# Optimization experiments

Hardware: AMD Instinct MI355X
Metric: run time of the kernel (lower is better)

## Reference

```python
import jax, jax.numpy as jnp
import numpy as np

N_NODES = 50000
N_EDGES = 800000
N_GRAPHS = 64
HID = 128
FEAT = 64
OUT = 32
N_LAYERS = 3
DECAY = 0.9
THRESH = 0.1


def setup_inputs() -> dict:
    key = jax.random.key(0)
    ks = jax.random.split(key, 24)
    s = 0.05
    inp = {
        "x": jax.random.normal(ks[0], (N_NODES, FEAT), jnp.float32),
        "edge_attr": jax.random.normal(ks[1], (N_EDGES, 1), jnp.float32),
        "initial_importance": jax.random.uniform(ks[2], (N_NODES, 1), jnp.float32),
        "imp_proj_W": jax.random.normal(ks[3], (1, HID), jnp.float32) * s,
        "imp_proj_b": jnp.zeros((HID,), jnp.float32),
        "init_W": jax.random.normal(ks[4], (FEAT + HID, HID), jnp.float32) * s,
        "init_b": jnp.zeros((HID,), jnp.float32),
        "msg_W": jax.random.normal(ks[5], (N_LAYERS, HID, HID), jnp.float32) * s,
        "msg_b": jnp.zeros((N_LAYERS, HID), jnp.float32),
        "upd_W": jax.random.normal(ks[6], (N_LAYERS, 2 * HID, HID), jnp.float32) * s,
        "upd_b": jnp.zeros((N_LAYERS, HID), jnp.float32),
        "gate_W": jax.random.normal(ks[7], (N_LAYERS, HID + 1, HID), jnp.float32) * s,
        "gate_b": jnp.zeros((N_LAYERS, HID), jnp.float32),
        "prop_W": jax.random.normal(ks[8], (N_LAYERS, HID, 1), jnp.float32) * s,
        "prop_b": jnp.zeros((N_LAYERS, 1), jnp.float32),
        "norm_w": jnp.ones((N_LAYERS, HID), jnp.float32),
        "norm_b": jnp.zeros((N_LAYERS, HID), jnp.float32),
        "norm_a": jnp.ones((N_LAYERS, HID), jnp.float32),
        "final_W": jax.random.normal(ks[9], (HID, OUT), jnp.float32) * s,
        "final_b": jnp.zeros((OUT,), jnp.float32),
        "edge_index": jax.random.randint(ks[10], (2, N_EDGES), 0, N_NODES, jnp.int32),
        # evenly spread sorted graph ids -> every graph non-empty
        "batch": (jnp.arange(N_NODES, dtype=jnp.int32) * N_GRAPHS) // N_NODES,
    }
    return inp


def _normalize_importance(imp, batch):
    # per-graph min/max normalization, fused segment reductions
    mn = jax.ops.segment_min(imp, batch, num_segments=N_GRAPHS)[batch]
    mx = jax.ops.segment_max(imp, batch, num_segments=N_GRAPHS)[batch]
    return (imp - mn) / (mx - mn + 1e-8)


def _graph_norm(x, batch, counts, w, b, a):
    # PyG GraphNorm: y = w * (x - a*mean) / sqrt(var(x - a*mean) + eps) + b
    mean = jax.ops.segment_sum(x, batch, num_segments=N_GRAPHS) / counts
    out = x - a * mean[batch]
    var = jax.ops.segment_sum(out * out, batch, num_segments=N_GRAPHS) / counts
    std = jnp.sqrt(var + 1e-5)
    return w * out / std[batch] + b


def _forward(x, edge_attr, initial_importance, imp_proj_W, imp_proj_b, init_W,
             init_b, msg_W, msg_b, upd_W, upd_b, gate_W, gate_b, prop_W, prop_b,
             norm_w, norm_b, norm_a, final_W, final_b, edge_index, batch):
    src, dst = edge_index[0], edge_index[1]
    counts = jax.ops.segment_sum(jnp.ones((N_NODES, 1), x.dtype), batch,
                                 num_segments=N_GRAPHS)  # [G,1]

    imp0 = initial_importance[:, 0]                       # [N]
    importance = _normalize_importance(imp0, batch)       # [N]
    imp_emb = importance[:, None] @ imp_proj_W + imp_proj_b  # [N,H]
    h = jnp.concatenate([x, imp_emb], axis=-1) @ init_W + init_b  # [N,H]

    for l in range(N_LAYERS):
        # MPNN: gather -> linear -> scatter-add -> update
        msg = h[src] @ msg_W[l] + msg_b[l]                # [E,H]
        aggr = jax.ops.segment_sum(msg, dst, num_segments=N_NODES)  # [N,H]
        conv = jnp.concatenate([h, aggr], axis=-1) @ upd_W[l] + upd_b[l]
        # importance gating
        gate_in = jnp.concatenate([conv, importance[:, None]], axis=-1)
        gate = jax.nn.sigmoid(gate_in @ gate_W[l] + gate_b[l])
        out = gate * conv + (1.0 - gate) * h
        prop = out @ prop_W[l] + prop_b[l]                # [N,1]
        # norm + relu (dropout p=0 in eval)
        h = jax.nn.relu(_graph_norm(out, batch, counts, norm_w[l], norm_b[l], norm_a[l]))
        # importance update
        imp = DECAY * importance + (1.0 - DECAY) * prop[:, 0]
        imp = _normalize_importance(imp, batch)
        imp = jnp.where(imp < THRESH, 0.0, imp)
        importance = _normalize_importance(imp, batch)

    h = h @ final_W + final_b                             # [N,OUT]
    logits = jax.ops.segment_sum(h, batch, num_segments=N_GRAPHS) / counts  # [G,OUT]
    final_importance = _normalize_importance(imp0 + importance, batch)
    return logits, final_importance[:, None]


def reference(x, edge_attr, initial_importance, imp_proj_W, imp_proj_b, init_W,
              init_b, msg_W, msg_b, upd_W, upd_b, gate_W, gate_b, prop_W, prop_b,
              norm_w, norm_b, norm_a, final_W, final_b, edge_index, batch):
    return _forward(x, edge_attr, initial_importance, imp_proj_W, imp_proj_b,
                    init_W, init_b, msg_W, msg_b, upd_W, upd_b, gate_W, gate_b,
                    prop_W, prop_b, norm_w, norm_b, norm_a, final_W, final_b,
                    edge_index, batch)
```

## Files before the change

### kernel.cpp

```cpp
#include <hip/hip_runtime.h>
#include <cstdint>

#define NN 50000
#define NE 800000
#define NG 64
#define HD 128
#define FT 64
#define NLAYERS 3
#define MB 32
#define NBLK 1563
#define AGN 64
#define AGB (8*((NN + AGN - 1)/AGN))

__global__ void k_gbounds(const int* __restrict__ batch, int* __restrict__ gstart){
    int i = blockIdx.x*blockDim.x + threadIdx.x;
    if (i >= NN) return;
    int g = batch[i];
    if (i == 0){ for (int q = 0; q <= g; ++q) gstart[q] = 0; }
    else { int gp = batch[i-1]; for (int q = gp+1; q <= g; ++q) gstart[q] = i; }
    if (i == NN-1){ for (int q = g+1; q <= NG; ++q) gstart[q] = NN; }
}

__device__ __forceinline__ void block_minmax(float lmn, float lmx, float* red,
                                             float& omn, float& omx){
    #pragma unroll
    for (int off = 32; off > 0; off >>= 1){
        lmn = fminf(lmn, __shfl_xor(lmn, off));
        lmx = fmaxf(lmx, __shfl_xor(lmx, off));
    }
    int wave = threadIdx.x >> 6;
    if ((threadIdx.x & 63) == 0){ red[wave] = lmn; red[4+wave] = lmx; }
    __syncthreads();
    omn = fminf(fminf(red[0], red[1]), fminf(red[2], red[3]));
    omx = fmaxf(fmaxf(red[4], red[5]), fmaxf(red[6], red[7]));
    __syncthreads();
}

__global__ __launch_bounds__(256) void k_norm_graph(
    const float* __restrict__ va, const int* __restrict__ gstart,
    float* __restrict__ out)
{
    __shared__ float sv[1024];
    __shared__ float red[8];
    int g = blockIdx.x;
    int s = gstart[g], n = gstart[g+1] - s;
    int tid = threadIdx.x;
    float lmn = 3.4e38f, lmx = -3.4e38f;
    for (int i = tid; i < n; i += 256){
        float v = va[s+i];
        sv[i] = v;
        lmn = fminf(lmn, v); lmx = fmaxf(lmx, v);
    }
    float lo, hi;
    block_minmax(lmn, lmx, red, lo, hi);
    float inv = 1.f/(hi - lo + 1e-8f);
    for (int i = tid; i < n; i += 256) out[s+i] = (sv[i] - lo)*inv;
}

__global__ void k_fold_init(const float* __restrict__ pW, const float* __restrict__ pb,
                            const float* __restrict__ iW, const float* __restrict__ ib,
                            float* __restrict__ W0, float* __restrict__ b0){
    int j = threadIdx.x;
    for (int k = 0; k < FT; ++k) W0[k*HD + j] = iW[k*HD + j];
    float w2 = 0.f, b2 = 0.f;
    for (int k = 0; k < HD; ++k){
        float w = iW[(FT + k)*HD + j];
        w2 += pW[k]*w;
        b2 += pb[k]*w;
    }
    W0[FT*HD + j] = w2;
    b0[j] = ib[j] + b2;
}

__global__ void k_fold_layer(const float* __restrict__ msgW, const float* __restrict__ updW,
                             const float* __restrict__ msgb,
                             float* __restrict__ WfA, float* __restrict__ bcvA){
    int l = blockIdx.y;
    const float* mW  = msgW + (size_t)l*HD*HD;
    const float* uW  = updW + (size_t)l*2*HD*HD;
    const float* mb  = msgb + (size_t)l*HD;
    float* Wf  = WfA  + (size_t)l*2*HD*HD;
    float* bcv = bcvA + (size_t)l*HD;
    int j = threadIdx.x;
    int r = blockIdx.x;
    if (r < HD){
        Wf[(size_t)r*HD + j] = uW[(size_t)r*HD + j];
    } else if (r < 2*HD){
        int rr = r - HD;
        const float* uWbot = uW + (size_t)HD*HD;
        float acc = 0.f;
        for (int k = 0; k < HD; ++k)
            acc = fmaf(mW[(size_t)rr*HD + k], uWbot[(size_t)k*HD + j], acc);
        Wf[(size_t)r*HD + j] = acc;
    } else {
        const float* uWbot = uW + (size_t)HD*HD;
        float acc = 0.f;
        for (int k = 0; k < HD; ++k)
            acc = fmaf(mb[k], uWbot[(size_t)k*HD + j], acc);
        bcv[j] = acc;
    }
}

__global__ __launch_bounds__(256) void k_init(
    const float* __restrict__ x, const float* __restrict__ imp,
    const float* __restrict__ W0, const float* __restrict__ b0v,
    float* __restrict__ h)
{
    __shared__ float lds[MB][FT];
    __shared__ float scs[MB];
    int base = blockIdx.x*MB, tid = threadIdx.x;
    #pragma unroll
    for (int i = 0; i < 2; ++i){
        int fidx = i*256 + tid;
        int t = fidx >> 4, c = fidx & 15;
        float4 v = {0.f,0.f,0.f,0.f};
        if (base + t < NN) v = *(const float4*)&x[(size_t)(base+t)*FT + c*4];
        *(float4*)&lds[t][c*4] = v;
    }
    if (tid < MB) scs[tid] = (base+tid < NN) ? imp[base+tid] : 0.f;
    __syncthreads();

    const int cg = tid & 31, rg = tid >> 5;
    const int c0 = cg*4, r0 = rg*4;
    const float4 wl4 = *(const float4*)&W0[(size_t)FT*HD + c0];
    const float4 b4  = *(const float4*)&b0v[c0];
    float acc[4][4];
    #pragma unroll
    for (int r = 0; r < 4; ++r){
        float s = scs[r0+r];
        acc[r][0] = fmaf(s, wl4.x, b4.x); acc[r][1] = fmaf(s, wl4.y, b4.y);
        acc[r][2] = fmaf(s, wl4.z, b4.z); acc[r][3] = fmaf(s, wl4.w, b4.w);
    }
    #pragma unroll 4
    for (int k4 = 0; k4 < 16; ++k4){
        const float4 w0 = *(const float4*)&W0[(size_t)(k4*4+0)*HD + c0];
        const float4 w1 = *(const float4*)&W0[(size_t)(k4*4+1)*HD + c0];
        const float4 w2 = *(const float4*)&W0[(size_t)(k4*4+2)*HD + c0];
        const float4 w3 = *(const float4*)&W0[(size_t)(k4*4+3)*HD + c0];
        #pragma unroll
        for (int r = 0; r < 4; ++r){
            const float4 a = *(const float4*)&lds[r0+r][k4*4];
            acc[r][0]=fmaf(a.x,w0.x,fmaf(a.y,w1.x,fmaf(a.z,w2.x,fmaf(a.w,w3.x,acc[r][0]))));
            acc[r][1]=fmaf(a.x,w0.y,fmaf(a.y,w1.y,fmaf(a.z,w2.y,fmaf(a.w,w3.y,acc[r][1]))));
            acc[r][2]=fmaf(a.x,w0.z,fmaf(a.y,w1.z,fmaf(a.z,w2.z,fmaf(a.w,w3.z,acc[r][2]))));
            acc[r][3]=fmaf(a.x,w0.w,fmaf(a.y,w1.w,fmaf(a.z,w2.w,fmaf(a.w,w3.w,acc[r][3]))));
        }
    }
    #pragma unroll
    for (int r = 0; r < 4; ++r)
        if (base + r0 + r < NN)
            *(float4*)&h[(size_t)(base+r0+r)*HD + c0] =
                make_float4(acc[r][0], acc[r][1], acc[r][2], acc[r][3]);
}

__global__ __launch_bounds__(256, 4) void k_layer(
    const float* __restrict__ h, const float* __restrict__ aggr,
    const float* __restrict__ imp, const int* __restrict__ deg,
    const float* __restrict__ Wf, const float* __restrict__ bcv,
    const float* __restrict__ ub,
    const float* __restrict__ gW, const float* __restrict__ gb,
    const float* __restrict__ prW, const float* __restrict__ prb,
    float* __restrict__ outbuf, float* __restrict__ ta)
{
    __shared__ float lds[MB][256];
    __shared__ float scs[MB];
    __shared__ float dgs[MB];
    __shared__ float red[8][4];
    const int base = blockIdx.x*MB, tid = threadIdx.x;

    #pragma unroll
    for (int i = 0; i < 8; ++i){
        int fidx = i*256 + tid;
        int t = fidx >> 6, c = fidx & 63;
        float4 v = {0.f,0.f,0.f,0.f};
        if (base + t < NN){
            const float* srcp = (c < 32) ? &h[(size_t)(base+t)*HD + c*4]
                                         : &aggr[(size_t)(base+t)*HD + (c-32)*4];
            v = *(const float4*)srcp;
        }
        *(float4*)&lds[t][c*4] = v;
    }
    if (tid < MB) scs[tid] = (base+tid < NN) ? imp[base+tid] : 0.f;
    else if (tid < 2*MB){
        int t = tid - MB;
        dgs[t] = (base+t < NN) ? (float)deg[base+t] : 0.f;
    }
    __syncthreads();

    const int cg = tid & 31, rg = tid >> 5;
    const int c0 = cg*4, r0 = rg*4;

    const float4 bc4 = *(const float4*)&bcv[c0];
    const float4 ub4 = *(const float4*)&ub[c0];
    float acc[4][4];
    #pragma unroll
    for (int r = 0; r < 4; ++r){
        float d = dgs[r0+r];
        acc[r][0] = fmaf(d, bc4.x, ub4.x); acc[r][1] = fmaf(d, bc4.y, ub4.y);
        acc[r][2] = fmaf(d, bc4.z, ub4.z); acc[r][3] = fmaf(d, bc4.w, ub4.w);
    }
    #pragma unroll 4
    for (int k4 = 0; k4 < 64; ++k4){
        const float4 w0 = *(const float4*)&Wf[(size_t)(k4*4+0)*HD + c0];
        const float4 w1 = *(const float4*)&Wf[(size_t)(k4*4+1)*HD + c0];
        const float4 w2 = *(const float4*)&Wf[(size_t)(k4*4+2)*HD + c0];
        const float4 w3 = *(const float4*)&Wf[(size_t)(k4*4+3)*HD + c0];
        #pragma unroll
        for (int r = 0; r < 4; ++r){
            const float4 a = *(const float4*)&lds[r0+r][k4*4];
            acc[r][0]=fmaf(a.x,w0.x,fmaf(a.y,w1.x,fmaf(a.z,w2.x,fmaf(a.w,w3.x,acc[r][0]))));
            acc[r][1]=fmaf(a.x,w0.y,fmaf(a.y,w1.y,fmaf(a.z,w2.y,fmaf(a.w,w3.y,acc[r][1]))));
            acc[r][2]=fmaf(a.x,w0.z,fmaf(a.y,w1.z,fmaf(a.z,w2.z,fmaf(a.w,w3.z,acc[r][2]))));
            acc[r][3]=fmaf(a.x,w0.w,fmaf(a.y,w1.w,fmaf(a.z,w2.w,fmaf(a.w,w3.w,acc[r][3]))));
        }
    }
    __syncthreads();
    #pragma unroll
    for (int r = 0; r < 4; ++r)
        *(float4*)&lds[r0+r][HD + c0] = make_float4(acc[r][0],acc[r][1],acc[r][2],acc[r][3]);
    __syncthreads();

    const float4 gwl = *(const float4*)&gW[(size_t)HD*HD + c0];
    const float4 gb4 = *(const float4*)&gb[c0];
    float z[4][4];
    #pragma unroll
    for (int r = 0; r < 4; ++r){
        float s = scs[r0+r];
        z[r][0] = fmaf(s, gwl.x, gb4.x); z[r][1] = fmaf(s, gwl.y, gb4.y);
        z[r][2] = fmaf(s, gwl.z, gb4.z); z[r][3] = fmaf(s, gwl.w, gb4.w);
    }
    #pragma unroll 4
    for (int k4 = 0; k4 < 32; ++k4){
        const float4 w0 = *(const float4*)&gW[(size_t)(k4*4+0)*HD + c0];
        const float4 w1 = *(const float4*)&gW[(size_t)(k4*4+1)*HD + c0];
        const float4 w2 = *(const float4*)&gW[(size_t)(k4*4+2)*HD + c0];
        const float4 w3 = *(const float4*)&gW[(size_t)(k4*4+3)*HD + c0];
        #pragma unroll
        for (int r = 0; r < 4; ++r){
            const float4 a = *(const float4*)&lds[r0+r][HD + k4*4];
            z[r][0]=fmaf(a.x,w0.x,fmaf(a.y,w1.x,fmaf(a.z,w2.x,fmaf(a.w,w3.x,z[r][0]))));
            z[r][1]=fmaf(a.x,w0.y,fmaf(a.y,w1.y,fmaf(a.z,w2.y,fmaf(a.w,w3.y,z[r][1]))));
            z[r][2]=fmaf(a.x,w0.z,fmaf(a.y,w1.z,fmaf(a.z,w2.z,fmaf(a.w,w3.z,z[r][2]))));
            z[r][3]=fmaf(a.x,w0.w,fmaf(a.y,w1.w,fmaf(a.z,w2.w,fmaf(a.w,w3.w,z[r][3]))));
        }
    }

    const float4 pr4 = *(const float4*)&prW[c0];
    float psum[4];
    #pragma unroll
    for (int r = 0; r < 4; ++r){
        const float4 hv = *(const float4*)&lds[r0+r][c0];
        float g0 = 1.f/(1.f + expf(-z[r][0]));
        float g1 = 1.f/(1.f + expf(-z[r][1]));
        float g2 = 1.f/(1.f + expf(-z[r][2]));
        float g3 = 1.f/(1.f + expf(-z[r][3]));
        float o0 = g0*acc[r][0] + (1.f-g0)*hv.x;
        float o1 = g1*acc[r][1] + (1.f-g1)*hv.y;
        float o2 = g2*acc[r][2] + (1.f-g2)*hv.z;
        float o3 = g3*acc[r][3] + (1.f-g3)*hv.w;
        if (base + r0 + r < NN)
            *(float4*)&outbuf[(size_t)(base+r0+r)*HD + c0] = make_float4(o0,o1,o2,o3);
        psum[r] = o0*pr4.x + o1*pr4.y + o2*pr4.z + o3*pr4.w;
    }
    #pragma unroll
    for (int r = 0; r < 4; ++r){
        float v = psum[r];
        #pragma unroll
        for (int off = 16; off > 0; off >>= 1) v += __shfl_xor(v, off);
        if (cg == 0) red[rg][r] = v;
    }
    __syncthreads();
    if (tid < MB && base + tid < NN)
        ta[base+tid] = 0.9f*scs[tid] + 0.1f*(red[tid>>2][tid&3] + prb[0]);
}

__global__ void k_deg(const int* __restrict__ dst, int* deg){
    int e = blockIdx.x*blockDim.x + threadIdx.x;
    if (e < NE) atomicAdd(&deg[dst[e]], 1);
}

__global__ __launch_bounds__(1024) void k_scan(const int* __restrict__ deg,
                                               int* __restrict__ rowstart){
    __shared__ int wtot[16];
    __shared__ int woff[16];
    __shared__ int carry;
    int tid = threadIdx.x, lane = tid & 63, wv = tid >> 6;
    if (tid == 0) carry = 0;
    __syncthreads();
    for (int base = 0; base < NN; base += 1024){
        int i = base + tid;
        int v = (i < NN) ? deg[i] : 0;
        int x = v;
        #pragma unroll
        for (int off = 1; off < 64; off <<= 1){
            int y = __shfl_up(x, off);
            if (lane >= off) x += y;
        }
        if (lane == 63) wtot[wv] = x;
        __syncthreads();
        if (tid == 0){
            int a = carry;
            for (int w2 = 0; w2 < 16; ++w2){ woff[w2] = a; a += wtot[w2]; }
            carry = a;
        }
        __syncthreads();
        if (i < NN) rowstart[i] = woff[wv] + x - v;
    }
    __syncthreads();
    if (tid == 0) rowstart[NN] = carry;
}

__global__ void k_copy_int(const int* __restrict__ a, int* __restrict__ b, int n){
    int i = blockIdx.x*blockDim.x + threadIdx.x;
    if (i < n) b[i] = a[i];
}

__global__ void k_fill(const int* __restrict__ src, const int* __restrict__ dst,
                       int* cursor, int* __restrict__ csr){
    int e = blockIdx.x*blockDim.x + threadIdx.x;
    if (e < NE){
        int d = dst[e];
        int p = atomicAdd(&cursor[d], 1);
        csr[p] = src[e];
    }
}

__global__ __launch_bounds__(256) void k_aggregate(
    const float* __restrict__ hm, const int* __restrict__ rowstart,
    const int* __restrict__ csr, float* __restrict__ aggr)
{
    int bid = blockIdx.x;
    int slice = bid & 7;
    int nb = bid >> 3;
    int node = nb*AGN + (threadIdx.x >> 2);
    if (node >= NN) return;
    int ln = threadIdx.x & 3;
    const float* __restrict__ hp = hm + (size_t)slice*16 + (size_t)ln*4;
    float4 a0 = {0.f,0.f,0.f,0.f}, a1 = a0, a2 = a0, a3 = a0;
    float4 a4 = a0, a5 = a0, a6 = a0, a7 = a0;
    int e0 = rowstart[node], e1 = rowstart[node+1];
    int e = e0;
    for (; e + 7 < e1; e += 8){
        int s0 = csr[e],   s1 = csr[e+1], s2 = csr[e+2], s3 = csr[e+3];
        int s4 = csr[e+4], s5 = csr[e+5], s6 = csr[e+6], s7 = csr[e+7];
        const float4 v0 = *(const float4*)&hp[(size_t)s0*HD];
        const float4 v1 = *(const float4*)&hp[(size_t)s1*HD];
        const float4 v2 = *(const float4*)&hp[(size_t)s2*HD];
        const float4 v3 = *(const float4*)&hp[(size_t)s3*HD];
        const float4 v4 = *(const float4*)&hp[(size_t)s4*HD];
        const float4 v5 = *(const float4*)&hp[(size_t)s5*HD];
        const float4 v6 = *(const float4*)&hp[(size_t)s6*HD];
        const float4 v7 = *(const float4*)&hp[(size_t)s7*HD];
        a0.x += v0.x; a0.y += v0.y; a0.z += v0.z; a0.w += v0.w;
        a1.x += v1.x; a1.y += v1.y; a1.z += v1.z; a1.w += v1.w;
        a2.x += v2.x; a2.y += v2.y; a2.z += v2.z; a2.w += v2.w;
        a3.x += v3.x; a3.y += v3.y; a3.z += v3.z; a3.w += v3.w;
        a4.x += v4.x; a4.y += v4.y; a4.z += v4.z; a4.w += v4.w;
        a5.x += v5.x; a5.y += v5.y; a5.z += v5.z; a5.w += v5.w;
        a6.x += v6.x; a6.y += v6.y; a6.z += v6.z; a6.w += v6.w;
        a7.x += v7.x; a7.y += v7.y; a7.z += v7.z; a7.w += v7.w;
    }
    for (; e + 3 < e1; e += 4){
        int s0 = csr[e], s1 = csr[e+1], s2 = csr[e+2], s3 = csr[e+3];
        const float4 v0 = *(const float4*)&hp[(size_t)s0*HD];
        const float4 v1 = *(const float4*)&hp[(size_t)s1*HD];
        const float4 v2 = *(const float4*)&hp[(size_t)s2*HD];
        const float4 v3 = *(const float4*)&hp[(size_t)s3*HD];
        a0.x += v0.x; a0.y += v0.y; a0.z += v0.z; a0.w += v0.w;
        a1.x += v1.x; a1.y += v1.y; a1.z += v1.z; a1.w += v1.w;
        a2.x += v2.x; a2.y += v2.y; a2.z += v2.z; a2.w += v2.w;
        a3.x += v3.x; a3.y += v3.y; a3.z += v3.z; a3.w += v3.w;
    }
    for (; e < e1; ++e){
        int s0 = csr[e];
        const float4 v0 = *(const float4*)&hp[(size_t)s0*HD];
        a0.x += v0.x; a0.y += v0.y; a0.z += v0.z; a0.w += v0.w;
    }
    a0.x += a1.x; a0.y += a1.y; a0.z += a1.z; a0.w += a1.w;
    a2.x += a3.x; a2.y += a3.y; a2.z += a3.z; a2.w += a3.w;
    a4.x += a5.x; a4.y += a5.y; a4.z += a5.z; a4.w += a5.w;
    a6.x += a7.x; a6.y += a7.y; a6.z += a7.z; a6.w += a7.w;
    a0.x += a2.x; a0.y += a2.y; a0.z += a2.z; a0.w += a2.w;
    a4.x += a6.x; a4.y += a6.y; a4.z += a6.z; a4.w += a6.w;
    a0.x += a4.x; a0.y += a4.y; a0.z += a4.z; a0.w += a4.w;
    *(float4*)&aggr[(size_t)node*HD + slice*16 + ln*4] = a0;
}

__global__ __launch_bounds__(256) void k_gnorm(
    const float* __restrict__ v, const int* __restrict__ gstart,
    const float* __restrict__ nw, const float* __restrict__ nb,
    const float* __restrict__ na, float* __restrict__ hout,
    const float* __restrict__ tsrc, float* __restrict__ tdst)
{
    int g = blockIdx.x;
    int part = blockIdx.y;
    int s = gstart[g], n = gstart[g+1] - s;
    int tid = threadIdx.x;

    if (part == 4){
        __shared__ float sv[1024];
        __shared__ float red[8];
        float lmn = 3.4e38f, lmx = -3.4e38f;
        for (int i = tid; i < n; i += 256){
            float val = tsrc[s+i]; sv[i] = val;
            lmn = fminf(lmn, val); lmx = fmaxf(lmx, val);
        }
        float lo, hi;
        block_minmax(lmn, lmx, red, lo, hi);
        float inv = 1.f/(hi - lo + 1e-8f);
        lmn = 3.4e38f; lmx = -3.4e38f;
        for (int i = tid; i < n; i += 256){
            float t2 = (sv[i] - lo)*inv;
            if (t2 < 0.1f) t2 = 0.f;
            sv[i] = t2;
            lmn = fminf(lmn, t2); lmx = fmaxf(lmx, t2);
        }
        float lo2, hi2;
        block_minmax(lmn, lmx, red, lo2, hi2);
        float inv2 = 1.f/(hi2 - lo2 + 1e-8f);
        for (int i = tid; i < n; i += 256) tdst[s+i] = (sv[i] - lo2)*inv2;
        return;
    }

    __shared__ float4 rs1[32][8];
    __shared__ float4 rs2[32][8];
    __shared__ float amv[32], scv[32], nbv[32];
    int rg = tid >> 3, c4l = tid & 7;
    size_t coff = (size_t)part*32 + c4l*4;
    float4 s1 = {0.f,0.f,0.f,0.f}, s2 = {0.f,0.f,0.f,0.f};
    for (int i = rg; i < n; i += 32){
        const float4 vv = *(const float4*)&v[(size_t)(s+i)*HD + coff];
        s1.x += vv.x; s1.y += vv.y; s1.z += vv.z; s1.w += vv.w;
        s2.x += vv.x*vv.x; s2.y += vv.y*vv.y; s2.z += vv.z*vv.z; s2.w += vv.w*vv.w;
    }
    rs1[rg][c4l] = s1; rs2[rg][c4l] = s2;
    __syncthreads();
    if (tid < 8){
        float4 t1 = {0.f,0.f,0.f,0.f}, t2 = {0.f,0.f,0.f,0.f};
        for (int r = 0; r < 32; ++r){
            float4 a = rs1[r][tid]; float4 b = rs2[r][tid];
            t1.x += a.x; t1.y += a.y; t1.z += a.z; t1.w += a.w;
            t2.x += b.x; t2.y += b.y; t2.z += b.z; t2.w += b.w;
        }
        float fn = (float)n;
        float S1[4] = {t1.x,t1.y,t1.z,t1.w};
        float S2[4] = {t2.x,t2.y,t2.z,t2.w};
        #pragma unroll
        for (int e = 0; e < 4; ++e){
            int j = part*32 + tid*4 + e;
            float m = S1[e]/fn;
            float aj = na[j];
            float var = S2[e]/fn - (2.f*aj - aj*aj)*m*m;
            float stdv = sqrtf(var + 1e-5f);
            amv[tid*4+e] = aj*m;
            scv[tid*4+e] = nw[j]/stdv;
            nbv[tid*4+e] = nb[j];
        }
    }
    __syncthreads();
    const float4 am4 = *(const float4*)&amv[c4l*4];
    const float4 sc4 = *(const float4*)&scv[c4l*4];
    const float4 nb4 = *(const float4*)&nbv[c4l*4];
    for (int i = rg; i < n; i += 32){
        const float4 vv = *(const float4*)&v[(size_t)(s+i)*HD + coff];
        float4 r;
        r.x = fmaxf((vv.x - am4.x)*sc4.x + nb4.x, 0.f);
        r.y = fmaxf((vv.y - am4.y)*sc4.y + nb4.y, 0.f);
        r.z = fmaxf((vv.z - am4.z)*sc4.z + nb4.z, 0.f);
        r.w = fmaxf((vv.w - am4.w)*sc4.w + nb4.w, 0.f);
        *(float4*)&hout[(size_t)(s+i)*HD + coff] = r;
    }
}

__global__ __launch_bounds__(1024) void k_logits(
    const float* __restrict__ h, const int* __restrict__ gstart,
    const float* __restrict__ fW, const float* __restrict__ fb,
    const float* __restrict__ imp0, const float* __restrict__ impf,
    float* __restrict__ outp)
{
    __shared__ float4 rs1[32][32];
    __shared__ float gsum[HD];
    __shared__ float redn[32];
    int g = blockIdx.x;
    int s = gstart[g], n = gstart[g+1] - s;
    int tid = threadIdx.x;
    int c4 = tid & 31, rg = tid >> 5;
    float4 s1 = {0.f,0.f,0.f,0.f};
    for (int i = rg; i < n; i += 32){
        const float4 vv = *(const float4*)&h[(size_t)(s+i)*HD + c4*4];
        s1.x += vv.x; s1.y += vv.y; s1.z += vv.z; s1.w += vv.w;
    }
    rs1[rg][c4] = s1;
    __syncthreads();
    if (tid < 32){
        float4 t1 = {0.f,0.f,0.f,0.f};
        for (int r = 0; r < 32; ++r){
            float4 a = rs1[r][tid];
            t1.x += a.x; t1.y += a.y; t1.z += a.z; t1.w += a.w;
        }
        gsum[tid*4+0] = t1.x; gsum[tid*4+1] = t1.y;
        gsum[tid*4+2] = t1.z; gsum[tid*4+3] = t1.w;
    }
    __syncthreads();
    if (tid < 32){
        int o = tid;
        float acc = 0.f;
        for (int k = 0; k < HD; ++k) acc = fmaf(gsum[k], fW[k*32 + o], acc);
        outp[g*32 + o] = acc/(float)n + fb[o];
    }
    float val = 0.f;
    bool has = (tid < n);
    float lmn = 3.4e38f, lmx = -3.4e38f;
    if (has){ val = imp0[s+tid] + impf[s+tid]; lmn = val; lmx = val; }
    #pragma unroll
    for (int off = 32; off > 0; off >>= 1){
        lmn = fminf(lmn, __shfl_xor(lmn, off));
        lmx = fmaxf(lmx, __shfl_xor(lmx, off));
    }
    int wv = tid >> 6, lane = tid & 63;
    if (lane == 0){ redn[wv] = lmn; redn[16+wv] = lmx; }
    __syncthreads();
    float lo = redn[0], hi = redn[16];
    for (int r2 = 1; r2 < 16; ++r2){
        lo = fminf(lo, redn[r2]); hi = fmaxf(hi, redn[16+r2]);
    }
    if (has) outp[NG*32 + s + tid] = (val - lo)/(hi - lo + 1e-8f);
}

extern "C" void kernel_launch(void* const* d_in, const int* in_sizes, int n_in,
                              void* d_out, int out_size, void* d_ws, size_t ws_size,
                              hipStream_t stream){
    const float* x    = (const float*)d_in[0];
    const float* imp0 = (const float*)d_in[2];
    const float* pW   = (const float*)d_in[3];
    const float* pb   = (const float*)d_in[4];
    const float* iW   = (const float*)d_in[5];
    const float* ib   = (const float*)d_in[6];
    const float* msgW = (const float*)d_in[7];
    const float* msgb = (const float*)d_in[8];
    const float* updW = (const float*)d_in[9];
    const float* updb = (const float*)d_in[10];
    const float* gWt  = (const float*)d_in[11];
    const float* gb   = (const float*)d_in[12];
    const float* prW  = (const float*)d_in[13];
    const float* prb  = (const float*)d_in[14];
    const float* nw   = (const float*)d_in[15];
    const float* nb   = (const float*)d_in[16];
    const float* na   = (const float*)d_in[17];
    const float* fW   = (const float*)d_in[18];
    const float* fb   = (const float*)d_in[19];
    const int* eidx   = (const int*)d_in[20];
    const int* batch  = (const int*)d_in[21];
    const int* esrc = eidx;
    const int* edst = eidx + NE;
    float* outp = (float*)d_out;

    char* w = (char*)d_ws;
    size_t off = 0;
    auto alloc = [&](size_t bytes)->char*{
        char* p = w + off;
        off += (bytes + 255) & ~(size_t)255;
        return p;
    };
    float* h     = (float*)alloc((size_t)NN*HD*4);
    float* aggB  = (float*)alloc((size_t)NN*HD*4);
    float* outA  = (float*)alloc((size_t)NN*HD*4);
    float* ta    = (float*)alloc((size_t)NN*4);
    float* imp   = (float*)alloc((size_t)NN*4);
    float* W0    = (float*)alloc((size_t)(FT+1)*HD*4);
    float* b0    = (float*)alloc((size_t)HD*4);
    float* Wf    = (float*)alloc((size_t)NLAYERS*2*HD*HD*4);
    float* bcv   = (float*)alloc((size_t)NLAYERS*HD*4);
    int* gstart  = (int*)alloc((size_t)(NG+1)*4);
    int* deg     = (int*)alloc((size_t)NN*4);
    int* rowst   = (int*)alloc((size_t)(NN+1)*4);
    int* cursor  = (int*)alloc((size_t)NN*4);
    int* csr     = (int*)alloc((size_t)NE*4);

    k_gbounds<<<196, 256, 0, stream>>>(batch, gstart);

    hipMemsetAsync(deg, 0, NN*4, stream);
    k_deg<<<3125, 256, 0, stream>>>(edst, deg);
    k_scan<<<1, 1024, 0, stream>>>(deg, rowst);
    k_copy_int<<<196, 256, 0, stream>>>(rowst, cursor, NN);
    k_fill<<<3125, 256, 0, stream>>>(esrc, edst, cursor, csr);

    k_fold_init<<<1, 128, 0, stream>>>(pW, pb, iW, ib, W0, b0);
    k_fold_layer<<<dim3(257, NLAYERS), 128, 0, stream>>>(msgW, updW, msgb, Wf, bcv);

    k_norm_graph<<<NG, 256, 0, stream>>>(imp0, gstart, imp);
    k_init<<<NBLK, 256, 0, stream>>>(x, imp, W0, b0, h);

    for (int l = 0; l < NLAYERS; ++l){
        k_aggregate<<<AGB, 256, 0, stream>>>(h, rowst, csr, aggB);
        k_layer<<<NBLK, 256, 0, stream>>>(
            h, aggB, imp, deg,
            Wf + (size_t)l*2*HD*HD, bcv + (size_t)l*HD,
            updb + (size_t)l*HD, gWt + (size_t)l*(HD+1)*HD, gb + (size_t)l*HD,
            prW + (size_t)l*HD, prb + l, outA, ta);
        k_gnorm<<<dim3(NG,5), 256, 0, stream>>>(outA, gstart,
            nw + (size_t)l*HD, nb + (size_t)l*HD, na + (size_t)l*HD, h, ta, imp);
    }

    k_logits<<<NG, 1024, 0, stream>>>(h, gstart, fW, fb, imp0, imp, outp);
}
```

Before: 763.1 us.

## Fuse neighbor aggregation into layer kernel, dropping the aggregate buffer

The separate CSR gather-sum kernel is removed and each k_layer block now gathers neighbor features for its 32 nodes straight into shared memory, with half-waves of 32 lanes each covering one full 128-float row. Degree is taken from the rowstart difference instead of the deg array. This avoids writing and re-reading a 50000x128 aggregate buffer and one launch per layer. In exchange, occupancy drops (launch bounds 4 to 3), the gather latency now sits in front of the GEMM within each block, and per-block load balance depends on node degree.

```diff
diff --git a/kernel.cpp b/kernel.cpp
--- a/kernel.cpp
+++ b/kernel.cpp
@@ -9,8 +9,6 @@
 #define NLAYERS 3
 #define MB 32
 #define NBLK 1563
-#define AGN 64
-#define AGB (8*((NN + AGN - 1)/AGN))
 
 __global__ void k_gbounds(const int* __restrict__ batch, int* __restrict__ gstart){
     int i = blockIdx.x*blockDim.x + threadIdx.x;
@@ -153,9 +151,10 @@
                 make_float4(acc[r][0], acc[r][1], acc[r][2], acc[r][3]);
 }
 
-__global__ __launch_bounds__(256, 4) void k_layer(
-    const float* __restrict__ h, const float* __restrict__ aggr,
-    const float* __restrict__ imp, const int* __restrict__ deg,
+__global__ __launch_bounds__(256, 3) void k_layer(
+    const float* __restrict__ h,
+    const int* __restrict__ rowst, const int* __restrict__ csr,
+    const float* __restrict__ imp,
     const float* __restrict__ Wf, const float* __restrict__ bcv,
     const float* __restrict__ ub,
     const float* __restrict__ gW, const float* __restrict__ gb,
@@ -169,21 +168,73 @@
     const int base = blockIdx.x*MB, tid = threadIdx.x;
 
     #pragma unroll
-    for (int i = 0; i < 8; ++i){
+    for (int i = 0; i < 4; ++i){
         int fidx = i*256 + tid;
-        int t = fidx >> 6, c = fidx & 63;
+        int t = fidx >> 5, c = fidx & 31;
         float4 v = {0.f,0.f,0.f,0.f};
-        if (base + t < NN){
-            const float* srcp = (c < 32) ? &h[(size_t)(base+t)*HD + c*4]
-                                         : &aggr[(size_t)(base+t)*HD + (c-32)*4];
-            v = *(const float4*)srcp;
-        }
+        if (base + t < NN) v = *(const float4*)&h[(size_t)(base+t)*HD + c*4];
         *(float4*)&lds[t][c*4] = v;
     }
     if (tid < MB) scs[tid] = (base+tid < NN) ? imp[base+tid] : 0.f;
-    else if (tid < 2*MB){
-        int t = tid - MB;
-        dgs[t] = (base+t < NN) ? (float)deg[base+t] : 0.f;
+
+    {
+        const int lane = tid & 31;
+        #pragma unroll
+        for (int pass = 0; pass < 4; ++pass){
+            const int t = pass*8 + (tid >> 5);
+            const int node = base + t;
+            float4 a0 = {0.f,0.f,0.f,0.f}, a1 = a0, a2 = a0, a3 = a0;
+            float4 a4 = a0, a5 = a0, a6 = a0, a7 = a0;
+            if (node < NN){
+                int e0 = rowst[node], e1 = rowst[node+1];
+                if (lane == 0) dgs[t] = (float)(e1 - e0);
+                int e = e0;
+                for (; e + 7 < e1; e += 8){
+                    int s0 = csr[e],   s1 = csr[e+1], s2 = csr[e+2], s3 = csr[e+3];
+                    int s4 = csr[e+4], s5 = csr[e+5], s6 = csr[e+6], s7 = csr[e+7];
+                    const float4 v0 = *(const float4*)&h[(size_t)s0*HD + lane*4];
+                    const float4 v1 = *(const float4*)&h[(size_t)s1*HD + lane*4];
+                    const float4 v2 = *(const float4*)&h[(size_t)s2*HD + lane*4];
+                    const float4 v3 = *(const float4*)&h[(size_t)s3*HD + lane*4];
+                    const float4 v4 = *(const float4*)&h[(size_t)s4*HD + lane*4];
+                    const float4 v5 = *(const float4*)&h[(size_t)s5*HD + lane*4];
+                    const float4 v6 = *(const float4*)&h[(size_t)s6*HD + lane*4];
+                    const float4 v7 = *(const float4*)&h[(size_t)s7*HD + lane*4];
+                    a0.x += v0.x; a0.y += v0.y; a0.z += v0.z; a0.w += v0.w;
+                    a1.x += v1.x; a1.y += v1.y; a1.z += v1.z; a1.w += v1.w;
+                    a2.x += v2.x; a2.y += v2.y; a2.z += v2.z; a2.w += v2.w;
+                    a3.x += v3.x; a3.y += v3.y; a3.z += v3.z; a3.w += v3.w;
+                    a4.x += v4.x; a4.y += v4.y; a4.z += v4.z; a4.w += v4.w;
+                    a5.x += v5.x; a5.y += v5.y; a5.z += v5.z; a5.w += v5.w;
+                    a6.x += v6.x; a6.y += v6.y; a6.z += v6.z; a6.w += v6.w;
+                    a7.x += v7.x; a7.y += v7.y; a7.z += v7.z; a7.w += v7.w;
+                }
+                for (; e + 3 < e1; e += 4){
+                    int s0 = csr[e], s1 = csr[e+1], s2 = csr[e+2], s3 = csr[e+3];
+                    const float4 v0 = *(const float4*)&h[(size_t)s0*HD + lane*4];
+                    const float4 v1 = *(const float4*)&h[(size_t)s1*HD + lane*4];
+                    const float4 v2 = *(const float4*)&h[(size_t)s2*HD + lane*4];
+                    const float4 v3 = *(const float4*)&h[(size_t)s3*HD + lane*4];
+                    a0.x += v0.x; a0.y += v0.y; a0.z += v0.z; a0.w += v0.w;
+                    a1.x += v1.x; a1.y += v1.y; a1.z += v1.z; a1.w += v1.w;
+                    a2.x += v2.x; a2.y += v2.y; a2.z += v2.z; a2.w += v2.w;
+                    a3.x += v3.x; a3.y += v3.y; a3.z += v3.z; a3.w += v3.w;
+                }
+                for (; e < e1; ++e){
+                    int s0 = csr[e];
+                    const float4 v0 = *(const float4*)&h[(size_t)s0*HD + lane*4];
+                    a0.x += v0.x; a0.y += v0.y; a0.z += v0.z; a0.w += v0.w;
+                }
+            } else if (lane == 0) dgs[t] = 0.f;
+            a0.x += a1.x; a0.y += a1.y; a0.z += a1.z; a0.w += a1.w;
+            a2.x += a3.x; a2.y += a3.y; a2.z += a3.z; a2.w += a3.w;
+            a4.x += a5.x; a4.y += a5.y; a4.z += a5.z; a4.w += a5.w;
+            a6.x += a7.x; a6.y += a7.y; a6.z += a7.z; a6.w += a7.w;
+            a0.x += a2.x; a0.y += a2.y; a0.z += a2.z; a0.w += a2.w;
+            a4.x += a6.x; a4.y += a6.y; a4.z += a6.z; a4.w += a6.w;
+            a0.x += a4.x; a0.y += a4.y; a0.z += a4.z; a0.w += a4.w;
+            *(float4*)&lds[t][HD + lane*4] = a0;
+        }
     }
     __syncthreads();
 
@@ -323,67 +374,6 @@
         int p = atomicAdd(&cursor[d], 1);
         csr[p] = src[e];
     }
-}
-
-__global__ __launch_bounds__(256) void k_aggregate(
-    const float* __restrict__ hm, const int* __restrict__ rowstart,
-    const int* __restrict__ csr, float* __restrict__ aggr)
-{
-    int bid = blockIdx.x;
-    int slice = bid & 7;
-    int nb = bid >> 3;
-    int node = nb*AGN + (threadIdx.x >> 2);
-    if (node >= NN) return;
-    int ln = threadIdx.x & 3;
-    const float* __restrict__ hp = hm + (size_t)slice*16 + (size_t)ln*4;
-    float4 a0 = {0.f,0.f,0.f,0.f}, a1 = a0, a2 = a0, a3 = a0;
-    float4 a4 = a0, a5 = a0, a6 = a0, a7 = a0;
-    int e0 = rowstart[node], e1 = rowstart[node+1];
-    int e = e0;
-    for (; e + 7 < e1; e += 8){
-        int s0 = csr[e],   s1 = csr[e+1], s2 = csr[e+2], s3 = csr[e+3];
-        int s4 = csr[e+4], s5 = csr[e+5], s6 = csr[e+6], s7 = csr[e+7];
-        const float4 v0 = *(const float4*)&hp[(size_t)s0*HD];
-        const float4 v1 = *(const float4*)&hp[(size_t)s1*HD];
-        const float4 v2 = *(const float4*)&hp[(size_t)s2*HD];
-        const float4 v3 = *(const float4*)&hp[(size_t)s3*HD];
-        const float4 v4 = *(const float4*)&hp[(size_t)s4*HD];
-        const float4 v5 = *(const float4*)&hp[(size_t)s5*HD];
-        const float4 v6 = *(const float4*)&hp[(size_t)s6*HD];
-        const float4 v7 = *(const float4*)&hp[(size_t)s7*HD];
-        a0.x += v0.x; a0.y += v0.y; a0.z += v0.z; a0.w += v0.w;
-        a1.x += v1.x; a1.y += v1.y; a1.z += v1.z; a1.w += v1.w;
-        a2.x += v2.x; a2.y += v2.y; a2.z += v2.z; a2.w += v2.w;
-        a3.x += v3.x; a3.y += v3.y; a3.z += v3.z; a3.w += v3.w;
-        a4.x += v4.x; a4.y += v4.y; a4.z += v4.z; a4.w += v4.w;
-        a5.x += v5.x; a5.y += v5.y; a5.z += v5.z; a5.w += v5.w;
-        a6.x += v6.x; a6.y += v6.y; a6.z += v6.z; a6.w += v6.w;
-        a7.x += v7.x; a7.y += v7.y; a7.z += v7.z; a7.w += v7.w;
-    }
-    for (; e + 3 < e1; e += 4){
-        int s0 = csr[e], s1 = csr[e+1], s2 = csr[e+2], s3 = csr[e+3];
-        const float4 v0 = *(const float4*)&hp[(size_t)s0*HD];
-        const float4 v1 = *(const float4*)&hp[(size_t)s1*HD];
-        const float4 v2 = *(const float4*)&hp[(size_t)s2*HD];
-        const float4 v3 = *(const float4*)&hp[(size_t)s3*HD];
-        a0.x += v0.x; a0.y += v0.y; a0.z += v0.z; a0.w += v0.w;
-        a1.x += v1.x; a1.y += v1.y; a1.z += v1.z; a1.w += v1.w;
-        a2.x += v2.x; a2.y += v2.y; a2.z += v2.z; a2.w += v2.w;
-        a3.x += v3.x; a3.y += v3.y; a3.z += v3.z; a3.w += v3.w;
-    }
-    for (; e < e1; ++e){
-        int s0 = csr[e];
-        const float4 v0 = *(const float4*)&hp[(size_t)s0*HD];
-        a0.x += v0.x; a0.y += v0.y; a0.z += v0.z; a0.w += v0.w;
-    }
-    a0.x += a1.x; a0.y += a1.y; a0.z += a1.z; a0.w += a1.w;
-    a2.x += a3.x; a2.y += a3.y; a2.z += a3.z; a2.w += a3.w;
-    a4.x += a5.x; a4.y += a5.y; a4.z += a5.z; a4.w += a5.w;
-    a6.x += a7.x; a6.y += a7.y; a6.z += a7.z; a6.w += a7.w;
-    a0.x += a2.x; a0.y += a2.y; a0.z += a2.z; a0.w += a2.w;
-    a4.x += a6.x; a4.y += a6.y; a4.z += a6.z; a4.w += a6.w;
-    a0.x += a4.x; a0.y += a4.y; a0.z += a4.z; a0.w += a4.w;
-    *(float4*)&aggr[(size_t)node*HD + slice*16 + ln*4] = a0;
 }
 
 __global__ __launch_bounds__(256) void k_gnorm(
@@ -563,7 +553,6 @@
         return p;
     };
     float* h     = (float*)alloc((size_t)NN*HD*4);
-    float* aggB  = (float*)alloc((size_t)NN*HD*4);
     float* outA  = (float*)alloc((size_t)NN*HD*4);
     float* ta    = (float*)alloc((size_t)NN*4);
     float* imp   = (float*)alloc((size_t)NN*4);
@@ -592,9 +581,8 @@
     k_init<<<NBLK, 256, 0, stream>>>(x, imp, W0, b0, h);
 
     for (int l = 0; l < NLAYERS; ++l){
-        k_aggregate<<<AGB, 256, 0, stream>>>(h, rowst, csr, aggB);
         k_layer<<<NBLK, 256, 0, stream>>>(
-            h, aggB, imp, deg,
+            h, rowst, csr, imp,
             Wf + (size_t)l*2*HD*HD, bcv + (size_t)l*HD,
             updb + (size_t)l*HD, gWt + (size_t)l*(HD+1)*HD, gb + (size_t)l*HD,
             prW + (size_t)l*HD, prb + l, outA, ta);
```

Result: faster. 689.5 us (-9.6%).
